# Optimization experiments

Hardware: AMD Instinct MI355X
Metric: run time of the kernel (lower is better)

The kernel has to match this reference:

```python
import jax, jax.numpy as jnp
import numpy as np

EPSILON = 1e-8
K = 3
PAD = K // 2


def setup_inputs() -> dict:
    key = jax.random.key(0)
    k1, k2, k3, k4 = jax.random.split(key, 4)
    B, FI, FO, H, W, DSTYLE = 8, 512, 512, 64, 64, 512
    return {
        "x": jax.random.normal(k1, (B, FI, H, W), dtype=jnp.float32),
        "style": jax.random.normal(k2, (B, DSTYLE), dtype=jnp.float32),
        "w": jax.random.normal(k3, (FO, FI, K, K), dtype=jnp.float32),
        "fc_w": jax.random.normal(k4, (FI, DSTYLE), dtype=jnp.float32),  # modLinear weight [dim_out=fi, dim_in=dim_style]
        "fc_b": jnp.zeros((FI,), dtype=jnp.float32),
    }


def reference(x, style, w, fc_w, fc_b):
    B, FI, H, W = x.shape
    FO = w.shape[0]
    DSTYLE = fc_w.shape[1]
    fc_scale = DSTYLE ** (-0.5)            # modLinear w_scale (lr_mult=1)
    w_scale = (FI * K * K) ** (-0.5)       # modConv w_scale

    # modLinear: style -> per-input-channel modulation s, shape [B, FI]
    s = style @ (fc_w * fc_scale).T + fc_b

    # Demod factor: d[b, fo] = rsqrt(sum_{fi,k,k} (w_scale * w * s[b,fi])^2 + eps)
    wsq = jnp.sum((w * w_scale) ** 2, axis=(2, 3))          # [FO, FI]
    d = jax.lax.rsqrt(jnp.einsum('of,bf->bo', wsq, s ** 2) + EPSILON)  # [B, FO]

    # Equivalent to per-sample grouped conv: scale input channels by s,
    # conv with shared base weight, scale output channels by demod.
    xm = x * s[:, :, None, None]
    y = jax.lax.conv_general_dilated(
        xm, w * w_scale,
        window_strides=(1, 1),
        padding=((PAD, PAD), (PAD, PAD)),
        dimension_numbers=('NCHW', 'OIHW', 'NCHW'),
    )
    return y * d[:, :, None, None]
```

## Files before the change

kernel.cpp:

```cpp
#include <hip/hip_runtime.h>


typedef __bf16 bf16_t;
typedef __bf16 bf16x8 __attribute__((ext_vector_type(8)));
typedef float floatx4 __attribute__((ext_vector_type(4)));

#define HW_ 4096
#define FCSCALE 0.04419417382415922f
#define WSCALE  0.014731391274719742f

__device__ __forceinline__ void gload_lds16(const bf16_t* g, bf16_t* l) {
  __builtin_amdgcn_global_load_lds(
      (const __attribute__((address_space(1))) void*)g,
      (__attribute__((address_space(3))) void*)l, 16, 0, 0);
}

__global__ void k_style(const float* __restrict__ style, const float* __restrict__ fc_w,
                        const float* __restrict__ fc_b, float* __restrict__ s_out) {
  int o = blockIdx.x * 4 + (threadIdx.x >> 6);
  int lane = threadIdx.x & 63;
  int b = o >> 9, fi = o & 511;
  const float4* st = (const float4*)(style + b * 512);
  const float4* fw = (const float4*)(fc_w + (size_t)fi * 512);
  float4 a0 = st[lane * 2],     w0 = fw[lane * 2];
  float4 a1 = st[lane * 2 + 1], w1 = fw[lane * 2 + 1];
  float acc = a0.x * w0.x + a0.y * w0.y + a0.z * w0.z + a0.w * w0.w
            + a1.x * w1.x + a1.y * w1.y + a1.z * w1.z + a1.w * w1.w;
#pragma unroll
  for (int d = 32; d >= 1; d >>= 1) acc += __shfl_xor(acc, d, 64);
  if (lane == 0) s_out[o] = acc * FCSCALE + fc_b[fi];
}

__global__ void k_wsq_wt(const float* __restrict__ w, float* __restrict__ wsq,
                         bf16_t* __restrict__ wt) {
  int idx = blockIdx.x * 256 + threadIdx.x;
  int fo = idx >> 9, fi = idx & 511;
  const float* wp = w + (size_t)idx * 9;
  float v[9], q = 0.f;
#pragma unroll
  for (int k = 0; k < 9; ++k) { v[k] = wp[k] * WSCALE; q += v[k] * v[k]; }
  wsq[idx] = q;
#pragma unroll
  for (int k = 0; k < 9; ++k)
    wt[((((size_t)k * 64) + (fi >> 3)) * 512 + fo) * 8 + (fi & 7)] = (bf16_t)v[k];
}

__global__ void k_demod(const float* __restrict__ wsq, const float* __restrict__ s,
                        float* __restrict__ dcoef) {
  int o = blockIdx.x * 4 + (threadIdx.x >> 6);
  int lane = threadIdx.x & 63;
  int b = o >> 9, fo = o & 511;
  const float4* wq = (const float4*)(wsq + (size_t)fo * 512);
  const float4* sp = (const float4*)(s + b * 512);
  float acc = 0.f;
#pragma unroll
  for (int i = 0; i < 2; ++i) {
    float4 q = wq[lane * 2 + i], sv = sp[lane * 2 + i];
    acc += q.x * sv.x * sv.x + q.y * sv.y * sv.y + q.z * sv.z * sv.z + q.w * sv.w * sv.w;
  }
#pragma unroll
  for (int d = 32; d >= 1; d >>= 1) acc += __shfl_xor(acc, d, 64);
  if (lane == 0) dcoef[o] = rsqrtf(acc + 1e-8f);
}

__global__ void k_modx(const float* __restrict__ x, const float* __restrict__ s,
                       bf16_t* __restrict__ xT) {
  __shared__ float tile[32][65];
  int b = blockIdx.z;
  int fi0 = blockIdx.x * 32;
  int h = blockIdx.y;
  int t = threadIdx.x;
  int c4 = (t & 15) * 4, fr = t >> 4;
#pragma unroll
  for (int i = 0; i < 2; ++i) {
    int fi_l = i * 16 + fr;
    float sv = s[b * 512 + fi0 + fi_l];
    float4 v = *(const float4*)(x + ((size_t)(b * 512 + fi0 + fi_l)) * HW_ + h * 64 + c4);
    tile[fi_l][c4] = v.x * sv; tile[fi_l][c4 + 1] = v.y * sv;
    tile[fi_l][c4 + 2] = v.z * sv; tile[fi_l][c4 + 3] = v.w * sv;
  }
  __syncthreads();
  int g_l = t >> 6, wcol = t & 63;
  bf16x8 vv;
#pragma unroll
  for (int j = 0; j < 8; ++j) vv[j] = (bf16_t)tile[g_l * 8 + j][wcol];
  *(bf16x8*)&xT[((((size_t)(b * 64 + h)) * 64 + (fi0 >> 3) + g_l) * 64 + wcol) * 8] = vv;
}

__global__ __launch_bounds__(256, 2) void k_conv(const bf16_t* __restrict__ wt,
                                                 const bf16_t* __restrict__ xT,
                                                 const float* __restrict__ dcoef,
                                                 const bf16_t* __restrict__ zerobuf,
                                                 float* __restrict__ out) {
  __shared__ __align__(16) bf16_t xls[2][4 * 256 * 8];
  __shared__ __align__(16) bf16_t wls[2][4 * 128 * 8];

  int b   = blockIdx.x;
  int foB = blockIdx.y;
  int hq  = blockIdx.z;
  int t = threadIdx.x;
  int wv = t >> 6, lane = t & 63, quad = lane >> 4, l16 = lane & 15;
  int h0 = hq * 4;
  int fo_l = t & 127, chunk_hi = t >> 7;

  const bf16_t* xTb = xT + (size_t)b * 64 * 64 * 64 * 8;

  floatx4 acc[8][4];
#pragma unroll
  for (int i = 0; i < 8; ++i)
#pragma unroll
    for (int j = 0; j < 4; ++j) acc[i][j] = (floatx4){0.f, 0.f, 0.f, 0.f};

  auto stage = [&](int it, int p) {
    int tap = it >> 4;
    int g0 = (it & 15) * 4;
    int kh = tap / 3, kw = tap - kh * 3;
    int rg = h0 + wv + kh - 1;
    int cg = lane + kw - 1;
    bool valid = ((unsigned)rg < 64u) && ((unsigned)cg < 64u);
#pragma unroll
    for (int itw = 0; itw < 2; ++itw) {
      int cw = itw * 2 + chunk_hi;
      gload_lds16(wt + ((((size_t)tap * 64) + g0 + cw) * 512 + foB * 128 + fo_l) * 8,
                  &wls[p][(itw * 256 + wv * 64) * 8]);
    }
#pragma unroll
    for (int it4 = 0; it4 < 4; ++it4) {
      const bf16_t* src = valid
          ? xTb + (((size_t)rg * 64 + g0 + it4) * 64 + cg) * 8
          : zerobuf;
      gload_lds16(src, &xls[p][(it4 * 256 + wv * 64) * 8]);
    }
  };

  stage(0, 0);

  for (int it = 0; it < 144; ++it) {
    int p = it & 1;
    __syncthreads();
    if (it + 1 < 144) stage(it + 1, p ^ 1);

    bf16x8 bfr[4];
#pragma unroll
    for (int j = 0; j < 4; ++j)
      bfr[j] = *(const bf16x8*)&xls[p][(quad * 256 + wv * 64 + j * 16 + l16) * 8];
#pragma unroll
    for (int i = 0; i < 8; ++i) {
      bf16x8 afr = *(const bf16x8*)&wls[p][(quad * 128 + i * 16 + l16) * 8];
#pragma unroll
      for (int j = 0; j < 4; ++j)
        acc[i][j] = __builtin_amdgcn_mfma_f32_16x16x32_bf16(afr, bfr[j], acc[i][j], 0, 0, 0);
    }
  }

  int h = h0 + wv;
#pragma unroll
  for (int i = 0; i < 8; ++i) {
#pragma unroll
    for (int rr = 0; rr < 4; ++rr) {
      int fo_g = foB * 128 + i * 16 + quad * 4 + rr;
      float dm = dcoef[b * 512 + fo_g];
      float* op = out + ((size_t)((b * 512 + fo_g) * 64 + h)) * 64;
#pragma unroll
      for (int j = 0; j < 4; ++j)
        op[j * 16 + l16] = acc[i][j][rr] * dm;
    }
  }
}

extern "C" void kernel_launch(void* const* d_in, const int* in_sizes, int n_in,
                              void* d_out, int out_size, void* d_ws, size_t ws_size,
                              hipStream_t stream) {
  const float* x     = (const float*)d_in[0];
  const float* style = (const float*)d_in[1];
  const float* w     = (const float*)d_in[2];
  const float* fc_w  = (const float*)d_in[3];
  const float* fc_b  = (const float*)d_in[4];
  float* out = (float*)d_out;
  char* ws = (char*)d_ws;

  float*  s       = (float*)(ws);
  float*  dcoef   = (float*)(ws + 16384);
  float*  wsq     = (float*)(ws + 32768);
  bf16_t* zerobuf = (bf16_t*)(ws + 1081344);
  bf16_t* wt      = (bf16_t*)(ws + 1081600);
  bf16_t* xT      = (bf16_t*)(ws + 5800192);

  hipMemsetAsync(zerobuf, 0, 256, stream);
  k_style<<<1024, 256, 0, stream>>>(style, fc_w, fc_b, s);
  k_wsq_wt<<<1024, 256, 0, stream>>>(w, wsq, wt);
  k_demod<<<1024, 256, 0, stream>>>(wsq, s, dcoef);
  k_modx<<<dim3(16, 64, 8), 256, 0, stream>>>(x, s, xT);
  k_conv<<<dim3(8, 4, 16), 256, 0, stream>>>(wt, xT, dcoef, zerobuf, out);
}
```

Measured before the change: 277.4 us.

## Triple-buffer conv LDS staging with explicit vmcnt waits and MFMA priority

Switches the conv main loop from double to triple buffering in LDS, issuing loads two iterations ahead. It replaces __syncthreads with partial s_waitcnt vmcnt plus raw barriers, so later prefetches stay in flight while the current stage computes. It also raises wave priority around the MFMA block. The cost is 50% more LDS (48KB per block), which may affect occupancy, and correctness depends on the hand-counted vmcnt values matching the 6 loads issued per stage.

```diff
diff --git a/kernel.cpp b/kernel.cpp
--- a/kernel.cpp
+++ b/kernel.cpp
@@ -92,8 +92,8 @@
                                                  const float* __restrict__ dcoef,
                                                  const bf16_t* __restrict__ zerobuf,
                                                  float* __restrict__ out) {
-  __shared__ __align__(16) bf16_t xls[2][4 * 256 * 8];
-  __shared__ __align__(16) bf16_t wls[2][4 * 128 * 8];
+  __shared__ __align__(16) bf16_t xls[3][4 * 256 * 8];
+  __shared__ __align__(16) bf16_t wls[3][4 * 128 * 8];
 
   int b   = blockIdx.x;
   int foB = blockIdx.y;
@@ -111,7 +111,7 @@
 #pragma unroll
     for (int j = 0; j < 4; ++j) acc[i][j] = (floatx4){0.f, 0.f, 0.f, 0.f};
 
-  auto stage = [&](int it, int p) {
+  auto stage = [&](int it, int pf) {
     int tap = it >> 4;
     int g0 = (it & 15) * 4;
     int kh = tap / 3, kw = tap - kh * 3;
@@ -122,36 +122,58 @@
     for (int itw = 0; itw < 2; ++itw) {
       int cw = itw * 2 + chunk_hi;
       gload_lds16(wt + ((((size_t)tap * 64) + g0 + cw) * 512 + foB * 128 + fo_l) * 8,
-                  &wls[p][(itw * 256 + wv * 64) * 8]);
+                  &wls[pf][(itw * 256 + wv * 64) * 8]);
     }
 #pragma unroll
     for (int it4 = 0; it4 < 4; ++it4) {
       const bf16_t* src = valid
           ? xTb + (((size_t)rg * 64 + g0 + it4) * 64 + cg) * 8
           : zerobuf;
-      gload_lds16(src, &xls[p][(it4 * 256 + wv * 64) * 8]);
+      gload_lds16(src, &xls[pf][(it4 * 256 + wv * 64) * 8]);
     }
   };
 
-  stage(0, 0);
-
-  for (int it = 0; it < 144; ++it) {
-    int p = it & 1;
-    __syncthreads();
-    if (it + 1 < 144) stage(it + 1, p ^ 1);
-
+  auto compute = [&](int pc) {
     bf16x8 bfr[4];
 #pragma unroll
     for (int j = 0; j < 4; ++j)
-      bfr[j] = *(const bf16x8*)&xls[p][(quad * 256 + wv * 64 + j * 16 + l16) * 8];
+      bfr[j] = *(const bf16x8*)&xls[pc][(quad * 256 + wv * 64 + j * 16 + l16) * 8];
+    __builtin_amdgcn_s_setprio(1);
 #pragma unroll
     for (int i = 0; i < 8; ++i) {
-      bf16x8 afr = *(const bf16x8*)&wls[p][(quad * 128 + i * 16 + l16) * 8];
+      bf16x8 afr = *(const bf16x8*)&wls[pc][(quad * 128 + i * 16 + l16) * 8];
 #pragma unroll
       for (int j = 0; j < 4; ++j)
         acc[i][j] = __builtin_amdgcn_mfma_f32_16x16x32_bf16(afr, bfr[j], acc[i][j], 0, 0, 0);
     }
-  }
+    __builtin_amdgcn_s_setprio(0);
+  };
+
+  stage(0, 0);
+  stage(1, 1);
+
+  int p = 0, pn = 2;
+  for (int it = 0; it < 142; ++it) {
+    stage(it + 2, pn);
+    asm volatile("s_waitcnt vmcnt(12)" ::: "memory");
+    __builtin_amdgcn_s_barrier();
+    __builtin_amdgcn_sched_barrier(0);
+    compute(p);
+    asm volatile("s_waitcnt lgkmcnt(0)" ::: "memory");
+    __builtin_amdgcn_s_barrier();
+    __builtin_amdgcn_sched_barrier(0);
+    p = (p == 2) ? 0 : p + 1;
+    pn = (pn == 2) ? 0 : pn + 1;
+  }
+  asm volatile("s_waitcnt vmcnt(6)" ::: "memory");
+  __builtin_amdgcn_s_barrier();
+  __builtin_amdgcn_sched_barrier(0);
+  compute(p);
+  p = (p == 2) ? 0 : p + 1;
+  asm volatile("s_waitcnt vmcnt(0)" ::: "memory");
+  __builtin_amdgcn_s_barrier();
+  __builtin_amdgcn_sched_barrier(0);
+  compute(p);
 
   int h = h0 + wv;
 #pragma unroll
```

Measured after the change: 271.1 us. 1.02x faster.
